# Optimization experiments

Measured on AMD Instinct MI355X. Metric: run time of the kernel, lower is better.

Reference implementation:

```python
import jax, jax.numpy as jnp
import numpy as np

N = 50000      # nodes
E = 800000     # edges
F_IN = 128     # usable node features (x has F_IN + 2 cols: mask, feats, dropped)
H = 3          # attention heads
C = 64         # hidden_channels (per-head out dim of GATConv)
NEG_SLOPE = 0.2  # PyG GATConv default leaky_relu slope


def setup_inputs() -> dict:
    key = jax.random.key(0)
    ks = jax.random.split(key, 13)
    s = 0.05
    x = jax.random.uniform(ks[0], (N, F_IN + 2), dtype=jnp.float32)
    edge_index = jax.random.randint(ks[1], (2, E), 0, N, dtype=jnp.int32)
    return {
        "x": x,
        "edge_index": edge_index,
        # commodity / toll embeddings (nn.Linear with bias)
        "W_com": jax.random.normal(ks[2], (F_IN, C), dtype=jnp.float32) * s,
        "b_com": jnp.zeros((C,), dtype=jnp.float32),
        "W_toll": jax.random.normal(ks[3], (F_IN, C), dtype=jnp.float32) * s,
        "b_toll": jnp.zeros((C,), dtype=jnp.float32),
        # GATConv: separate src/dst linears (bias=False in PyG), att vectors, out bias
        "W_src": jax.random.normal(ks[4], (C, H * C), dtype=jnp.float32) * s,
        "W_dst": jax.random.normal(ks[5], (C, H * C), dtype=jnp.float32) * s,
        "att_src": jax.random.normal(ks[6], (H, C), dtype=jnp.float32) * s,
        "att_dst": jax.random.normal(ks[7], (H, C), dtype=jnp.float32) * s,
        "bias_conv": jnp.zeros((H * C,), dtype=jnp.float32),
        # final lin1: (H*C) -> 1
        "W_lin1": jax.random.normal(ks[8], (H * C, 1), dtype=jnp.float32) * s,
        "b_lin1": jnp.zeros((1,), dtype=jnp.float32),
    }


def reference(x, edge_index, W_com, b_com, W_toll, b_toll,
              W_src, W_dst, att_src, att_dst, bias_conv, W_lin1, b_lin1):
    m = x[:, 0:1]                      # [N,1] mask column
    xf = x[:, 1:-1]                    # [N,F_IN]
    # masked mix of two embeddings, then relu
    h = jax.nn.relu((xf @ W_com + b_com) * (1.0 - m) + (xf @ W_toll + b_toll) * m)  # [N,C]
    # GATConv (heads=H, no self loops)
    hs = (h @ W_src).reshape(-1, H, C)  # source-transformed feats [N,H,C]
    hd = (h @ W_dst).reshape(-1, H, C)  # dest-transformed feats  [N,H,C]
    a_s = jnp.sum(hs * att_src, axis=-1)  # [N,H]
    a_d = jnp.sum(hd * att_dst, axis=-1)  # [N,H]
    src, dst = edge_index[0], edge_index[1]
    e = jax.nn.leaky_relu(a_s[src] + a_d[dst], NEG_SLOPE)  # [E,H]
    # segment softmax over incoming edges of each destination node
    mx = jax.ops.segment_max(e, dst, num_segments=N)       # [N,H]
    mx = jnp.where(jnp.isfinite(mx), mx, 0.0)
    ee = jnp.exp(e - mx[dst])
    denom = jax.ops.segment_sum(ee, dst, num_segments=N)   # [N,H]
    alpha = ee / (denom[dst] + 1e-16)                       # [E,H]
    # weighted scatter-aggregate of source messages
    msg = alpha[:, :, None] * hs[src]                       # [E,H,C]
    out = jax.ops.segment_sum(msg, dst, num_segments=N).reshape(-1, H * C) + bias_conv  # [N,H*C]
    y = (out @ W_lin1 + b_lin1).squeeze(1) * x[:, 0]        # [N]
    return y
```

## Files before the change

### kernel.cpp

```cpp
#include <hip/hip_runtime.h>
#include <hip/hip_fp16.h>
#include <math.h>

#define NN 50000
#define EE 800000
#define FIN 128
#define HH 3
#define CC 64
#define NEG_SLOPE 0.2f
#define XROW (FIN + 2)
#define SLOTS 48
#define NBUCK 256
#define BNODES 196
#define SORT_E 4096
#define SORT_BLKS 196
#define NODEB 782

typedef _Float16 f16x8 __attribute__((ext_vector_type(8)));
typedef float f32x4 __attribute__((ext_vector_type(4)));
typedef float f32x4u __attribute__((ext_vector_type(4), aligned(4)));

__global__ __launch_bounds__(1024) void k_sort(const int* __restrict__ ei,
                                               const float* __restrict__ W_com,
                                               const float* __restrict__ W_toll,
                                               const float* __restrict__ W_src,
                                               const float* __restrict__ att_src,
                                               const float* __restrict__ W_dst,
                                               const float* __restrict__ att_dst,
                                               const float* __restrict__ bias_conv,
                                               const float* __restrict__ W_lin1,
                                               const float* __restrict__ b_lin1,
                                               unsigned int* __restrict__ meta,
                                               unsigned int* __restrict__ buck,
                                               uint4* __restrict__ WcP,
                                               uint4* __restrict__ WtP,
                                               uint4* __restrict__ WqP,
                                               float* __restrict__ ybias) {
    __shared__ __align__(16) char smem[20480];
    const int b = blockIdx.x;
    const int t = threadIdx.x;

    if (b < SORT_BLKS) {
        unsigned int* se = (unsigned int*)smem;
        int* lcnt = (int*)(smem + 16384);
        int* sc   = lcnt + 256;
        int* loff = sc + 256;
        int* lcur = loff + 256;
        const int base = b * SORT_E;
        const int n = (EE - base < SORT_E) ? (EE - base) : SORT_E;

        if (t < NBUCK) lcnt[t] = 0;
        __syncthreads();

        unsigned int ev[4];
        int eb[4];
        #pragma unroll
        for (int i = 0; i < 4; ++i) {
            int idx = base + i * 1024 + t;
            if (idx < EE) {
                int s = ei[idx];
                int d = ei[EE + idx];
                ev[i] = ((unsigned int)d << 16) | (unsigned int)s;
                eb[i] = d / BNODES;
                atomicAdd(&lcnt[eb[i]], 1);
            } else {
                eb[i] = -1;
            }
        }
        __syncthreads();

        if (t < NBUCK) sc[t] = lcnt[t];
        __syncthreads();
        for (int off = 1; off < NBUCK; off <<= 1) {
            int v = (t < NBUCK && t >= off) ? sc[t - off] : 0;
            __syncthreads();
            if (t < NBUCK) sc[t] += v;
            __syncthreads();
        }
        if (t < NBUCK) {
            int c = lcnt[t];
            int lo = sc[t] - c;
            loff[t] = lo;
            lcur[t] = lo;
            meta[t * SORT_BLKS + b] = ((unsigned int)lo << 16) | (unsigned int)c;
        }
        __syncthreads();

        #pragma unroll
        for (int i = 0; i < 4; ++i) {
            if (eb[i] >= 0) {
                int p = atomicAdd(&lcur[eb[i]], 1);
                se[p] = ev[i];
            }
        }
        __syncthreads();

        for (int j = t; j < n; j += 1024)
            buck[base + j] = se[j];
        return;
    }

    if (b == SORT_BLKS) {
        if (t < 1024) {
            int e = t;
            int l = e & 63, kt = (e >> 6) & 3, ct = e >> 8;
            int kbase = kt * 32 + (l >> 4) * 8;
            int col = ct * 16 + (l & 15);
            f16x8 pc, pt;
            #pragma unroll
            for (int i = 0; i < 8; ++i) {
                pc[i] = (_Float16)W_com[(size_t)(kbase + i) * CC + col];
                pt[i] = (_Float16)W_toll[(size_t)(kbase + i) * CC + col];
            }
            WcP[e] = __builtin_bit_cast(uint4, pc);
            WtP[e] = __builtin_bit_cast(uint4, pt);
        }
        return;
    }

    float* Vl = (float*)smem;
    {
        int k = t >> 4, j = t & 15;
        float s = 0.f;
        if (j < 9) {
            const float* W = (j >= 3 && j < 6) ? W_dst : W_src;
            int head = (j < 3) ? j : ((j < 6) ? j - 3 : j - 6);
            const float* v = (j < 3) ? (att_src + head * CC)
                           : ((j < 6) ? (att_dst + head * CC)
                                      : (W_lin1 + head * CC));
            #pragma unroll 8
            for (int c = 0; c < CC; ++c)
                s = fmaf(W[(size_t)k * (HH * CC) + head * CC + c], v[c], s);
        }
        Vl[t] = s;
    }
    __syncthreads();
    if (t < 128) {
        int l = t & 63, kt = t >> 6;
        int kbase = kt * 32 + (l >> 4) * 8;
        int col = l & 15;
        f16x8 ps;
        #pragma unroll
        for (int i = 0; i < 8; ++i)
            ps[i] = (_Float16)Vl[(kbase + i) * 16 + col];
        WqP[kt * 64 + l] = __builtin_bit_cast(uint4, ps);
    }
    if (t == 128) {
        float s = b_lin1[0];
        for (int ch = 0; ch < HH * CC; ++ch)
            s = fmaf(bias_conv[ch], W_lin1[ch], s);
        ybias[0] = s;
    }
}

__global__ __launch_bounds__(256, 4) void k_main(const float* __restrict__ x,
                                                 const float* __restrict__ b_com,
                                                 const float* __restrict__ b_toll,
                                                 const uint4* __restrict__ WcP,
                                                 const uint4* __restrict__ WtP,
                                                 const uint4* __restrict__ WqP,
                                                 const unsigned int* __restrict__ meta,
                                                 const unsigned int* __restrict__ buck,
                                                 int* __restrict__ cnt,
                                                 unsigned short* __restrict__ ssrc,
                                                 float* __restrict__ rec_src,
                                                 float* __restrict__ rec_dst) {
    __shared__ __align__(16) char smem[19712];
    const int t = threadIdx.x;

    if (blockIdx.x >= NODEB) {
        const int bb = blockIdx.x - NODEB;
        int* lcnt = (int*)smem;
        uint4* lslv = (uint4*)(smem + 896);
        unsigned short* lsl = (unsigned short*)lslv;
        const int base = bb * BNODES;
        if (t < BNODES) lcnt[t] = 0;
        __syncthreads();
        if (t < SORT_BLKS) {
            unsigned int m = meta[bb * SORT_BLKS + t];
            int lo = (int)(m >> 16);
            int c = (int)(m & 0xFFFFu);
            const unsigned int* seg = buck + t * SORT_E + lo;
            for (int k = 0; k < c; ++k) {
                unsigned int u = seg[k];
                int dl = (int)(u >> 16) - base;
                int p = atomicAdd(&lcnt[dl], 1);
                if (p < SLOTS) lsl[dl * SLOTS + p] = (unsigned short)(u & 0xFFFFu);
            }
        }
        __syncthreads();
        int nvalid = NN - base;
        if (nvalid > BNODES) nvalid = BNODES;
        if (nvalid < 0) nvalid = 0;
        if (t < nvalid) cnt[base + t] = lcnt[t];
        uint4* dst = (uint4*)(ssrc + (size_t)base * SLOTS);
        int nchunks = nvalid * (SLOTS * 2 / 16);
        for (int i = t; i < nchunks; i += 256)
            dst[i] = lslv[i];
        return;
    }

    const int lane = t & 63;
    const int w = t >> 6;
    const int n0 = (blockIdx.x * 4 + w) * 16;
    if (n0 >= NN) return;
    _Float16* Hl = (_Float16*)(smem + w * 3072);
    float* Rl = (float*)(smem + w * 3072 + 2304);
    const int r16 = lane & 15;
    const int kg = lane >> 4;

    f16x8 xa[4];
    float m_own;
    {
        const float* xrow = x + (size_t)(n0 + r16) * XROW;
        m_own = xrow[0];
        const float* xr = xrow + 1 + kg * 8;
        #pragma unroll
        for (int kt = 0; kt < 4; ++kt) {
            f32x4u lo = *(const f32x4u*)(xr + kt * 32);
            f32x4u hi = *(const f32x4u*)(xr + kt * 32 + 4);
            f16x8 v;
            v[0] = (_Float16)lo.x; v[1] = (_Float16)lo.y;
            v[2] = (_Float16)lo.z; v[3] = (_Float16)lo.w;
            v[4] = (_Float16)hi.x; v[5] = (_Float16)hi.y;
            v[6] = (_Float16)hi.z; v[7] = (_Float16)hi.w;
            xa[kt] = v;
        }
    }
    float mr[4];
    #pragma unroll
    for (int r = 0; r < 4; ++r)
        mr[r] = __shfl(m_own, w * 64 + kg * 4 + r, 64);

    f32x4 accC[4], accT[4];
    #pragma unroll
    for (int ct = 0; ct < 4; ++ct) {
        float bc = b_com[ct * 16 + r16];
        float bt = b_toll[ct * 16 + r16];
        accC[ct] = (f32x4){bc, bc, bc, bc};
        accT[ct] = (f32x4){bt, bt, bt, bt};
    }
    {
        uint4 wc[4], wt[4], wcn[4], wtn[4];
        #pragma unroll
        for (int kt = 0; kt < 4; ++kt) {
            wc[kt] = WcP[kt * 64 + lane];
            wt[kt] = WtP[kt * 64 + lane];
        }
        #pragma unroll
        for (int ct = 0; ct < 4; ++ct) {
            if (ct < 3) {
                #pragma unroll
                for (int kt = 0; kt < 4; ++kt) {
                    wcn[kt] = WcP[((ct + 1) * 4 + kt) * 64 + lane];
                    wtn[kt] = WtP[((ct + 1) * 4 + kt) * 64 + lane];
                }
            }
            #pragma unroll
            for (int kt = 0; kt < 4; ++kt) {
                accC[ct] = __builtin_amdgcn_mfma_f32_16x16x32_f16(
                    xa[kt], __builtin_bit_cast(f16x8, wc[kt]), accC[ct], 0, 0, 0);
                accT[ct] = __builtin_amdgcn_mfma_f32_16x16x32_f16(
                    xa[kt], __builtin_bit_cast(f16x8, wt[kt]), accT[ct], 0, 0, 0);
            }
            #pragma unroll
            for (int kt = 0; kt < 4; ++kt) { wc[kt] = wcn[kt]; wt[kt] = wtn[kt]; }
        }
    }

    #pragma unroll
    for (int ct = 0; ct < 4; ++ct) {
        #pragma unroll
        for (int r = 0; r < 4; ++r) {
            float v = accC[ct][r] * (1.f - mr[r]) + accT[ct][r] * mr[r];
            Hl[(kg * 4 + r) * 72 + ct * 16 + r16] = (_Float16)(v > 0.f ? v : 0.f);
        }
    }

    f16x8 ha0 = *(const f16x8*)&Hl[r16 * 72 + kg * 8];
    f16x8 ha1 = *(const f16x8*)&Hl[r16 * 72 + 32 + kg * 8];
    {
        f32x4 acc = (f32x4){0.f, 0.f, 0.f, 0.f};
        acc = __builtin_amdgcn_mfma_f32_16x16x32_f16(
            ha0, __builtin_bit_cast(f16x8, WqP[lane]), acc, 0, 0, 0);
        acc = __builtin_amdgcn_mfma_f32_16x16x32_f16(
            ha1, __builtin_bit_cast(f16x8, WqP[64 + lane]), acc, 0, 0, 0);
        if (r16 < 9) {
            #pragma unroll
            for (int r = 0; r < 4; ++r)
                Rl[(kg * 4 + r) * 12 + r16] = acc[r];
        }
    }

    {
        int n = lane >> 2, q = lane & 3;
        const float* rn = &Rl[n * 12];
        float2 v;
        if (q == 0)      v = make_float2(rn[0], rn[1]);
        else if (q == 1) v = make_float2(rn[2], 0.f);
        else if (q == 2) v = make_float2(rn[6], rn[7]);
        else             v = make_float2(rn[8], 0.f);
        *(float2*)(rec_src + (size_t)(n0 + n) * 8 + q * 2) = v;
        float d = (q < 3) ? rn[3 + q] : 0.f;
        rec_dst[(size_t)(n0 + n) * 4 + q] = d;
    }
}

__global__ __launch_bounds__(256) void k_agg(const int* __restrict__ cnt,
                                             const unsigned short* __restrict__ ssrc,
                                             const float* __restrict__ rec_src,
                                             const float* __restrict__ rec_dst,
                                             const float* __restrict__ ybias,
                                             const float* __restrict__ x,
                                             float* __restrict__ y) {
    const int tid = threadIdx.x;
    const int node = blockIdx.x * 16 + (tid >> 4);
    const int sub = tid & 15;

    const float4 rd = *(const float4*)(rec_dst + (size_t)node * 4);
    int dg = cnt[node];
    if (dg > SLOTS) dg = SLOTS;
    const size_t off = (size_t)node * SLOTS;

    float n0 = 0.f, n1 = 0.f, n2 = 0.f;
    float d0 = 0.f, d1 = 0.f, d2 = 0.f;
    for (int j = sub; j < dg; j += 16) {
        unsigned sj = ssrc[off + j];
        const float4 A = *(const float4*)(rec_src + (size_t)sj * 8);
        const float4 Z = *(const float4*)(rec_src + (size_t)sj * 8 + 4);
        float e0 = A.x + rd.x; e0 = e0 > 0.f ? e0 : NEG_SLOPE * e0;
        float e1 = A.y + rd.y; e1 = e1 > 0.f ? e1 : NEG_SLOPE * e1;
        float e2 = A.z + rd.z; e2 = e2 > 0.f ? e2 : NEG_SLOPE * e2;
        float w0 = __expf(e0), w1 = __expf(e1), w2 = __expf(e2);
        d0 += w0; d1 += w1; d2 += w2;
        n0 = fmaf(w0, Z.x, n0);
        n1 = fmaf(w1, Z.y, n1);
        n2 = fmaf(w2, Z.z, n2);
    }
    #pragma unroll
    for (int o = 8; o > 0; o >>= 1) {
        n0 += __shfl_xor(n0, o, 16);
        n1 += __shfl_xor(n1, o, 16);
        n2 += __shfl_xor(n2, o, 16);
        d0 += __shfl_xor(d0, o, 16);
        d1 += __shfl_xor(d1, o, 16);
        d2 += __shfl_xor(d2, o, 16);
    }
    if (sub == 0) {
        float s = n0 / (d0 + 1e-16f) + n1 / (d1 + 1e-16f) + n2 / (d2 + 1e-16f)
                + ybias[0];
        y[node] = s * x[(size_t)node * XROW];
    }
}

extern "C" void kernel_launch(void* const* d_in, const int* in_sizes, int n_in,
                              void* d_out, int out_size, void* d_ws, size_t ws_size,
                              hipStream_t stream) {
    const float* x        = (const float*)d_in[0];
    const int*   ei       = (const int*)d_in[1];
    const float* W_com    = (const float*)d_in[2];
    const float* b_com    = (const float*)d_in[3];
    const float* W_toll   = (const float*)d_in[4];
    const float* b_toll   = (const float*)d_in[5];
    const float* W_src    = (const float*)d_in[6];
    const float* W_dst    = (const float*)d_in[7];
    const float* att_src  = (const float*)d_in[8];
    const float* att_dst  = (const float*)d_in[9];
    const float* bias_conv= (const float*)d_in[10];
    const float* W_lin1   = (const float*)d_in[11];
    const float* b_lin1   = (const float*)d_in[12];
    float* y = (float*)d_out;

    float* ws = (float*)d_ws;
    float* rec_src = ws;
    float* rec_dst = ws + 400000;
    float* ybias   = rec_dst + 200000;
    int* cnt  = (int*)(ybias + 256);
    unsigned int* meta = (unsigned int*)(cnt + NN);
    unsigned short* ssrc = (unsigned short*)(meta + 50432);
    unsigned int* buck = (unsigned int*)((int*)(meta + 50432) + 1200000);
    uint4* WcP = (uint4*)(buck + EE);
    uint4* WtP = WcP + 1024;
    uint4* WqP = WtP + 1024;

    k_sort<<<SORT_BLKS + 2, 1024, 0, stream>>>(ei, W_com, W_toll, W_src,
                                               att_src, W_dst, att_dst,
                                               bias_conv, W_lin1, b_lin1,
                                               meta, buck, WcP, WtP, WqP, ybias);
    k_main<<<NODEB + NBUCK, 256, 0, stream>>>(x, b_com, b_toll, WcP, WtP, WqP,
                                              meta, buck, cnt, ssrc,
                                              rec_src, rec_dst);
    k_agg<<<NN / 16, 256, 0, stream>>>(cnt, ssrc, rec_src, rec_dst, ybias, x, y);
}
```

Baseline: 47.68 us.

## Fuse bucket CSR build into aggregation kernel, keeping adjacency in LDS

The per-destination bucket scatter (building counts and source slots) moves out of k_main into a new aggregation kernel, which builds the slot lists in shared memory and then aggregates directly from them. This removes the global round trip of cnt/ssrc and the separate x read in the aggregation, since the mask value is now packed into the spare fourth slot of rec_dst. The trade-off is that aggregation now runs on only 256 blocks instead of about 3125, so parallelism is reduced and the serial bucket insertion can no longer overlap with the node transform.

```diff
diff --git a/kernel.cpp b/kernel.cpp
--- a/kernel.cpp
+++ b/kernel.cpp
@@ -159,47 +159,10 @@
                                                  const uint4* __restrict__ WcP,
                                                  const uint4* __restrict__ WtP,
                                                  const uint4* __restrict__ WqP,
-                                                 const unsigned int* __restrict__ meta,
-                                                 const unsigned int* __restrict__ buck,
-                                                 int* __restrict__ cnt,
-                                                 unsigned short* __restrict__ ssrc,
                                                  float* __restrict__ rec_src,
                                                  float* __restrict__ rec_dst) {
-    __shared__ __align__(16) char smem[19712];
+    __shared__ __align__(16) char smem[12288];
     const int t = threadIdx.x;
-
-    if (blockIdx.x >= NODEB) {
-        const int bb = blockIdx.x - NODEB;
-        int* lcnt = (int*)smem;
-        uint4* lslv = (uint4*)(smem + 896);
-        unsigned short* lsl = (unsigned short*)lslv;
-        const int base = bb * BNODES;
-        if (t < BNODES) lcnt[t] = 0;
-        __syncthreads();
-        if (t < SORT_BLKS) {
-            unsigned int m = meta[bb * SORT_BLKS + t];
-            int lo = (int)(m >> 16);
-            int c = (int)(m & 0xFFFFu);
-            const unsigned int* seg = buck + t * SORT_E + lo;
-            for (int k = 0; k < c; ++k) {
-                unsigned int u = seg[k];
-                int dl = (int)(u >> 16) - base;
-                int p = atomicAdd(&lcnt[dl], 1);
-                if (p < SLOTS) lsl[dl * SLOTS + p] = (unsigned short)(u & 0xFFFFu);
-            }
-        }
-        __syncthreads();
-        int nvalid = NN - base;
-        if (nvalid > BNODES) nvalid = BNODES;
-        if (nvalid < 0) nvalid = 0;
-        if (t < nvalid) cnt[base + t] = lcnt[t];
-        uint4* dst = (uint4*)(ssrc + (size_t)base * SLOTS);
-        int nchunks = nvalid * (SLOTS * 2 / 16);
-        for (int i = t; i < nchunks; i += 256)
-            dst[i] = lslv[i];
-        return;
-    }
-
     const int lane = t & 63;
     const int w = t >> 6;
     const int n0 = (blockIdx.x * 4 + w) * 16;
@@ -294,6 +257,7 @@
 
     {
         int n = lane >> 2, q = lane & 3;
+        float mm = __shfl(m_own, w * 64 + n, 64);
         const float* rn = &Rl[n * 12];
         float2 v;
         if (q == 0)      v = make_float2(rn[0], rn[1]);
@@ -301,55 +265,82 @@
         else if (q == 2) v = make_float2(rn[6], rn[7]);
         else             v = make_float2(rn[8], 0.f);
         *(float2*)(rec_src + (size_t)(n0 + n) * 8 + q * 2) = v;
-        float d = (q < 3) ? rn[3 + q] : 0.f;
+        float d = (q < 3) ? rn[3 + q] : mm;
         rec_dst[(size_t)(n0 + n) * 4 + q] = d;
     }
 }
 
-__global__ __launch_bounds__(256) void k_agg(const int* __restrict__ cnt,
-                                             const unsigned short* __restrict__ ssrc,
-                                             const float* __restrict__ rec_src,
-                                             const float* __restrict__ rec_dst,
-                                             const float* __restrict__ ybias,
-                                             const float* __restrict__ x,
-                                             float* __restrict__ y) {
-    const int tid = threadIdx.x;
-    const int node = blockIdx.x * 16 + (tid >> 4);
-    const int sub = tid & 15;
-
-    const float4 rd = *(const float4*)(rec_dst + (size_t)node * 4);
-    int dg = cnt[node];
-    if (dg > SLOTS) dg = SLOTS;
-    const size_t off = (size_t)node * SLOTS;
-
-    float n0 = 0.f, n1 = 0.f, n2 = 0.f;
-    float d0 = 0.f, d1 = 0.f, d2 = 0.f;
-    for (int j = sub; j < dg; j += 16) {
-        unsigned sj = ssrc[off + j];
-        const float4 A = *(const float4*)(rec_src + (size_t)sj * 8);
-        const float4 Z = *(const float4*)(rec_src + (size_t)sj * 8 + 4);
-        float e0 = A.x + rd.x; e0 = e0 > 0.f ? e0 : NEG_SLOPE * e0;
-        float e1 = A.y + rd.y; e1 = e1 > 0.f ? e1 : NEG_SLOPE * e1;
-        float e2 = A.z + rd.z; e2 = e2 > 0.f ? e2 : NEG_SLOPE * e2;
-        float w0 = __expf(e0), w1 = __expf(e1), w2 = __expf(e2);
-        d0 += w0; d1 += w1; d2 += w2;
-        n0 = fmaf(w0, Z.x, n0);
-        n1 = fmaf(w1, Z.y, n1);
-        n2 = fmaf(w2, Z.z, n2);
-    }
-    #pragma unroll
-    for (int o = 8; o > 0; o >>= 1) {
-        n0 += __shfl_xor(n0, o, 16);
-        n1 += __shfl_xor(n1, o, 16);
-        n2 += __shfl_xor(n2, o, 16);
-        d0 += __shfl_xor(d0, o, 16);
-        d1 += __shfl_xor(d1, o, 16);
-        d2 += __shfl_xor(d2, o, 16);
-    }
-    if (sub == 0) {
-        float s = n0 / (d0 + 1e-16f) + n1 / (d1 + 1e-16f) + n2 / (d2 + 1e-16f)
-                + ybias[0];
-        y[node] = s * x[(size_t)node * XROW];
+__global__ __launch_bounds__(256) void k_bagg(const unsigned int* __restrict__ meta,
+                                              const unsigned int* __restrict__ buck,
+                                              const float* __restrict__ rec_src,
+                                              const float* __restrict__ rec_dst,
+                                              const float* __restrict__ ybias,
+                                              float* __restrict__ y) {
+    __shared__ int lcnt[200];
+    __shared__ unsigned short lsl[BNODES * SLOTS];
+    const int bb = blockIdx.x;
+    const int t = threadIdx.x;
+    const int base = bb * BNODES;
+
+    if (t < BNODES) lcnt[t] = 0;
+    __syncthreads();
+    if (t < SORT_BLKS) {
+        unsigned int m = meta[bb * SORT_BLKS + t];
+        int lo = (int)(m >> 16);
+        int c = (int)(m & 0xFFFFu);
+        const unsigned int* seg = buck + t * SORT_E + lo;
+        for (int k = 0; k < c; ++k) {
+            unsigned int u = seg[k];
+            int dl = (int)(u >> 16) - base;
+            int p = atomicAdd(&lcnt[dl], 1);
+            if (p < SLOTS) lsl[dl * SLOTS + p] = (unsigned short)(u & 0xFFFFu);
+        }
+    }
+    __syncthreads();
+
+    int nvalid = NN - base;
+    if (nvalid > BNODES) nvalid = BNODES;
+    if (nvalid < 0) nvalid = 0;
+    const int grp = t >> 4;
+    const int sub = t & 15;
+    const float yb = ybias[0];
+
+    for (int nl = grp; nl < BNODES; nl += 16) {
+        if (nl >= nvalid) break;
+        const int node = base + nl;
+        const float4 rd = *(const float4*)(rec_dst + (size_t)node * 4);
+        int dg = lcnt[nl];
+        if (dg > SLOTS) dg = SLOTS;
+
+        float n0 = 0.f, n1 = 0.f, n2 = 0.f;
+        float d0 = 0.f, d1 = 0.f, d2 = 0.f;
+        for (int j = sub; j < dg; j += 16) {
+            unsigned sj = lsl[nl * SLOTS + j];
+            const float4 A = *(const float4*)(rec_src + (size_t)sj * 8);
+            const float4 Z = *(const float4*)(rec_src + (size_t)sj * 8 + 4);
+            float e0 = A.x + rd.x; e0 = e0 > 0.f ? e0 : NEG_SLOPE * e0;
+            float e1 = A.y + rd.y; e1 = e1 > 0.f ? e1 : NEG_SLOPE * e1;
+            float e2 = A.z + rd.z; e2 = e2 > 0.f ? e2 : NEG_SLOPE * e2;
+            float w0 = __expf(e0), w1 = __expf(e1), w2 = __expf(e2);
+            d0 += w0; d1 += w1; d2 += w2;
+            n0 = fmaf(w0, Z.x, n0);
+            n1 = fmaf(w1, Z.y, n1);
+            n2 = fmaf(w2, Z.z, n2);
+        }
+        #pragma unroll
+        for (int o = 8; o > 0; o >>= 1) {
+            n0 += __shfl_xor(n0, o, 16);
+            n1 += __shfl_xor(n1, o, 16);
+            n2 += __shfl_xor(n2, o, 16);
+            d0 += __shfl_xor(d0, o, 16);
+            d1 += __shfl_xor(d1, o, 16);
+            d2 += __shfl_xor(d2, o, 16);
+        }
+        if (sub == 0) {
+            float s = n0 / (d0 + 1e-16f) + n1 / (d1 + 1e-16f)
+                    + n2 / (d2 + 1e-16f) + yb;
+            y[node] = s * rd.w;
+        }
     }
 }
 
@@ -375,10 +366,8 @@
     float* rec_src = ws;
     float* rec_dst = ws + 400000;
     float* ybias   = rec_dst + 200000;
-    int* cnt  = (int*)(ybias + 256);
-    unsigned int* meta = (unsigned int*)(cnt + NN);
-    unsigned short* ssrc = (unsigned short*)(meta + 50432);
-    unsigned int* buck = (unsigned int*)((int*)(meta + 50432) + 1200000);
+    unsigned int* meta = (unsigned int*)(ybias + 256);
+    unsigned int* buck = meta + 50432;
     uint4* WcP = (uint4*)(buck + EE);
     uint4* WtP = WcP + 1024;
     uint4* WqP = WtP + 1024;
@@ -387,8 +376,7 @@
                                                att_src, W_dst, att_dst,
                                                bias_conv, W_lin1, b_lin1,
                                                meta, buck, WcP, WtP, WqP, ybias);
-    k_main<<<NODEB + NBUCK, 256, 0, stream>>>(x, b_com, b_toll, WcP, WtP, WqP,
-                                              meta, buck, cnt, ssrc,
-                                              rec_src, rec_dst);
-    k_agg<<<NN / 16, 256, 0, stream>>>(cnt, ssrc, rec_src, rec_dst, ybias, x, y);
+    k_main<<<NODEB, 256, 0, stream>>>(x, b_com, b_toll, WcP, WtP, WqP,
+                                      rec_src, rec_dst);
+    k_bagg<<<NBUCK, 256, 0, stream>>>(meta, buck, rec_src, rec_dst, ybias, y);
 }
```

New measurement: 58.06 us. +21.8%, slower.
